# Performance work log

Measured on AMD Instinct MI355X. Metric: run time of the kernel, lower is better.

Reference implementation:

```python
import jax, jax.numpy as jnp
import numpy as np

TEMPERATURE = 0.2
EPS = 1e-12  # F.normalize clamp eps


def setup_inputs() -> dict:
    key = jax.random.key(0)
    k1, k2 = jax.random.split(key)
    N, D = 4096, 256
    Z_1 = jax.random.normal(k1, (N, D), dtype=jnp.float32)
    Z_2 = jax.random.normal(k2, (N, D), dtype=jnp.float32)
    return {"Z_1": Z_1, "Z_2": Z_2}


def reference(Z_1, Z_2):
    N = Z_1.shape[0]
    M = 2 * N
    # concat views and L2-normalize rows (torch F.normalize semantics)
    Z = jnp.concatenate([Z_1, Z_2], axis=0)  # [2N, D]
    Z = Z / jnp.maximum(jnp.linalg.norm(Z, axis=1, keepdims=True), EPS)
    # full similarity matrix [2N, 2N]
    sim = jnp.matmul(Z, Z.T) / TEMPERATURE
    # positive for row i is column (i + N) mod 2N (other view of same sample,
    # identity diagonal discarded as in create_contrastive_masks)
    idx = jnp.arange(M)
    pos = sim[idx, (idx + N) % M]  # [2N]
    # logits = [pos, negatives]; label = 0 => CE = logsumexp(pos U negs) - pos.
    # pos U negs = all columns except the identity diagonal.
    diag = idx[:, None] == idx[None, :]
    sim_masked = jnp.where(diag, -jnp.inf, sim)
    lse = jax.nn.logsumexp(sim_masked, axis=1)  # [2N]
    return jnp.mean(lse - pos)
```

## Files before the change

kernel.cpp:

```cpp
#include <hip/hip_runtime.h>
#include <cstdint>
#include <cstddef>

#define TINV 5.0f
#define C5L2E 7.2134752044448170f
#define NROWS 4096
#define DDIM 256
#define MM 8192

typedef __bf16 bf16x8 __attribute__((ext_vector_type(8)));
typedef float f32x4 __attribute__((ext_vector_type(4)));

typedef const void __attribute__((address_space(1)))* gas_ptr;
typedef void __attribute__((address_space(3)))* las_ptr;

__global__ __launch_bounds__(256, 2)
void nrm_kernel(const float* __restrict__ Z1, const float* __restrict__ Z2,
                unsigned short* __restrict__ Zb, float* __restrict__ rowsumAcc) {
    if (blockIdx.x < 32) rowsumAcc[blockIdx.x * 256 + threadIdx.x] = 0.f;
    const int w = threadIdx.x >> 6, lane = threadIdx.x & 63;
    const int row = blockIdx.x * 4 + w;
    const float* src = row < NROWS ? Z1 + (size_t)row * DDIM
                                   : Z2 + (size_t)(row - NROWS) * DDIM;
    float4 v = reinterpret_cast<const float4*>(src)[lane];
    float ss = v.x*v.x + v.y*v.y + v.z*v.z + v.w*v.w;
    #pragma unroll
    for (int m = 1; m < 64; m <<= 1) ss += __shfl_xor(ss, m, 64);
    float inv = 1.0f / fmaxf(sqrtf(ss), 1e-12f);
    float o[4] = { v.x*inv, v.y*inv, v.z*inv, v.w*inv };
    unsigned short us[4];
    #pragma unroll
    for (int e = 0; e < 4; ++e) {
        unsigned int b = __builtin_bit_cast(unsigned int, o[e]);
        b += 0x7FFFu + ((b >> 16) & 1u);
        us[e] = (unsigned short)(b >> 16);
    }
    reinterpret_cast<ushort4*>(Zb + (size_t)row * DDIM)[lane] =
        *reinterpret_cast<ushort4*>(us);
}

__device__ __forceinline__ void stage32(const unsigned short* Zb, char* ldsdst,
                                        int rowStart, int tid) {
    const char* base = reinterpret_cast<const char*>(Zb) + (size_t)rowStart * 512;
    #pragma unroll
    for (int it = 0; it < 8; ++it) {
        int L = it * 4096 + tid * 16;
        int row = L >> 9;
        int soff = row * 512 + ((L & 511) ^ ((row & 15) << 4));
        __builtin_amdgcn_global_load_lds((gas_ptr)(base + soff), (las_ptr)(ldsdst + L),
                                         16, 0, 0);
    }
}

__global__ __launch_bounds__(256, 2)
void sim_lse_kernel(const unsigned short* __restrict__ Zb,
                    float* __restrict__ rowsumAcc,
                    float* __restrict__ posArr) {
    __shared__ char lds[65536];
    __shared__ float colPartLds[4][8][64];
    const int tid = threadIdx.x;
    const int lane = tid & 63;
    const int w = tid >> 6;
    const int r15 = lane & 15, hi = lane >> 4;
    const int r = blockIdx.x >> 3;
    const int s = blockIdx.x & 7;
    const int e0 = r & 7, e1 = e0 ^ 4;
    const int nt = 8 + ((s == e0) || (s == e1));
    const int extraHalf = (s == e1) ? 1 : 0;
    const int R0 = r * 128;

    if (s == 0) {
        colPartLds[w][0][lane] = 0.f;
        colPartLds[w][1][lane] = 0.f;
    }

    int koff[8];
    #pragma unroll
    for (int kk = 0; kk < 8; ++kk)
        koff[kk] = ((hi << 4) | (kk << 6)) ^ (r15 << 4);

    stage32(Zb, lds, R0, tid);
    stage32(Zb, lds + 32768, R0 + 64, tid);
    __syncthreads();
    bf16x8 qf[2][8];
    {
        const char* ab = lds + ((w >> 1) << 15);
        #pragma unroll
        for (int mf = 0; mf < 2; ++mf)
            #pragma unroll
            for (int kk = 0; kk < 8; ++kk)
                qf[mf][kk] = *reinterpret_cast<const bf16x8*>(
                    ab + ((w & 1) * 32 + mf * 16 + r15) * 512 + koff[kk]);
    }
    __syncthreads();

    int baddr[8];
    #pragma unroll
    for (int kk = 0; kk < 8; ++kk) baddr[kk] = r15 * 512 + koff[kk];

    float rowsum[2][4] = {{0,0,0,0},{0,0,0,0}};
    const int iBase = R0 + w * 32 + (hi << 2);

    auto colOf = [&](int t) -> int {
        int d = (t < 8) ? (s + ((t >> 1) << 3)) : 32;
        int half = (t < 8) ? (t & 1) : extraHalf;
        return ((r + d) & 63) * 128 + half * 64;
    };

    stage32(Zb, lds, colOf(0), tid);

    for (int t = 0; t < nt; ++t) {
        const int C0 = colOf(t);
        const int cur = (t & 1) << 15;
        if (t < nt - 1) {
            stage32(Zb, lds + (cur ^ 32768), colOf(t + 1), tid);
            asm volatile("s_waitcnt vmcnt(8)" ::: "memory");
        } else {
            asm volatile("s_waitcnt vmcnt(0)" ::: "memory");
        }
        __builtin_amdgcn_s_barrier();
        __builtin_amdgcn_sched_barrier(0);

        const int mode = (t == 8) ? 2 : ((s == 0 && t < 2) ? 1 : 0);
        #pragma unroll
        for (int nf = 0; nf < 4; ++nf) {
            f32x4 acc0 = {0,0,0,0}, acc1 = {0,0,0,0};
            #pragma unroll
            for (int kk = 0; kk < 8; ++kk) {
                bf16x8 b = *reinterpret_cast<const bf16x8*>(lds + cur + nf * 8192 + baddr[kk]);
                acc0 = __builtin_amdgcn_mfma_f32_16x16x32_bf16(qf[0][kk], b, acc0, 0, 0, 0);
                acc1 = __builtin_amdgcn_mfma_f32_16x16x32_bf16(qf[1][kk], b, acc1, 0, 0, 0);
            }
            const int j = C0 + nf * 16 + r15;
            if (mode == 0) {
                float s8 = 0.f;
                #pragma unroll
                for (int mf = 0; mf < 2; ++mf) {
                    const f32x4 a = mf ? acc1 : acc0;
                    #pragma unroll
                    for (int rr = 0; rr < 4; ++rr) {
                        float e = __builtin_amdgcn_exp2f(fmaf(a[rr], C5L2E, -C5L2E));
                        rowsum[mf][rr] += e;
                        s8 += e;
                    }
                }
                s8 += __shfl_xor(s8, 16, 64);
                s8 += __shfl_xor(s8, 32, 64);
                if (hi == 0) colPartLds[w][t][(t & 1) * 0 + nf * 16 + r15] = s8;
            } else if (mode == 1) {
                #pragma unroll
                for (int mf = 0; mf < 2; ++mf) {
                    const f32x4 a = mf ? acc1 : acc0;
                    #pragma unroll
                    for (int rr = 0; rr < 4; ++rr) {
                        const int i = iBase + mf * 16 + rr;
                        if (j != i)
                            rowsum[mf][rr] += __builtin_amdgcn_exp2f(fmaf(a[rr], C5L2E, -C5L2E));
                    }
                }
            } else {
                #pragma unroll
                for (int mf = 0; mf < 2; ++mf) {
                    const f32x4 a = mf ? acc1 : acc0;
                    #pragma unroll
                    for (int rr = 0; rr < 4; ++rr) {
                        const int i = iBase + mf * 16 + rr;
                        rowsum[mf][rr] += __builtin_amdgcn_exp2f(fmaf(a[rr], C5L2E, -C5L2E));
                        if (j == (i ^ 4096)) posArr[i] = a[rr] * TINV;
                    }
                }
            }
        }
        asm volatile("" ::: "memory");
        __builtin_amdgcn_sched_barrier(0);
        __builtin_amdgcn_s_barrier();
    }

    __syncthreads();
    #pragma unroll
    for (int z = 0; z < 2; ++z) {
        const int idx = z * 256 + tid;
        const int tt = idx >> 6, c = idx & 63;
        float v = colPartLds[0][tt][c] + colPartLds[1][tt][c]
                + colPartLds[2][tt][c] + colPartLds[3][tt][c];
        if (v != 0.f) atomicAdd(&rowsumAcc[colOf(tt) + c], v);
    }

    #pragma unroll
    for (int mf = 0; mf < 2; ++mf)
        #pragma unroll
        for (int rr = 0; rr < 4; ++rr) {
            float v = rowsum[mf][rr];
            v += __shfl_xor(v, 1, 64);
            v += __shfl_xor(v, 2, 64);
            v += __shfl_xor(v, 4, 64);
            v += __shfl_xor(v, 8, 64);
            if (r15 == 0) atomicAdd(&rowsumAcc[iBase + mf * 16 + rr], v);
        }
}

__global__ __launch_bounds__(128)
void fin1_kernel(const float* __restrict__ rowsumAcc, const float* __restrict__ posArr,
                 float* __restrict__ blockSums) {
    const int tid = threadIdx.x;
    const int i = blockIdx.x * 128 + tid;
    double v = (double)(logf(rowsumAcc[i]) + 5.0f - posArr[i]);
    #pragma unroll
    for (int m = 1; m < 64; m <<= 1) v += __shfl_xor(v, m, 64);
    __shared__ double red[2];
    if ((tid & 63) == 0) red[tid >> 6] = v;
    __syncthreads();
    if (tid == 0) blockSums[blockIdx.x] = (float)(red[0] + red[1]);
}

__global__ __launch_bounds__(64)
void fin2_kernel(const float* __restrict__ blockSums, float* __restrict__ out) {
    double v = (double)blockSums[threadIdx.x];
    #pragma unroll
    for (int m = 1; m < 64; m <<= 1) v += __shfl_xor(v, m, 64);
    if (threadIdx.x == 0) out[0] = (float)(v / (double)MM);
}

extern "C" void kernel_launch(void* const* d_in, const int* in_sizes, int n_in,
                              void* d_out, int out_size, void* d_ws, size_t ws_size,
                              hipStream_t stream) {
    const float* Z1 = (const float*)d_in[0];
    const float* Z2 = (const float*)d_in[1];
    float* out = (float*)d_out;
    char* ws = (char*)d_ws;
    unsigned short* Zb = (unsigned short*)ws;
    float* posArr = (float*)(ws + 4194304);
    float* rowsumAcc = (float*)(ws + 4194304 + 32768);
    float* blockSums = (float*)(ws + 4194304 + 65536);

    nrm_kernel<<<MM / 4, 256, 0, stream>>>(Z1, Z2, Zb, rowsumAcc);
    sim_lse_kernel<<<64 * 8, 256, 0, stream>>>(Zb, rowsumAcc, posArr);
    fin1_kernel<<<64, 128, 0, stream>>>(rowsumAcc, posArr, blockSums);
    fin2_kernel<<<1, 64, 0, stream>>>(blockSums, out);
}
```

Before: 43.31 us.

## Retile waves to 2x2 grid with 64-row A fragments held in AGPRs

Changes the per-wave tile from 32 rows by 64 columns to 64 rows by 32 columns, arranged as a 2x2 wave grid. Each B fragment loaded from LDS now feeds four MFMAs instead of two, halving LDS reads per MFMA. The A operand (query fragments) is doubled and pinned to AGPRs through inline asm to relieve VGPR pressure. Column partial sums are reduced across two waves instead of four. The risk is higher register use under the two-blocks-per-CU launch bound, and inline asm hides the MFMA dependencies from the compiler's scheduler.

```diff
diff --git a/kernel.cpp b/kernel.cpp
--- a/kernel.cpp
+++ b/kernel.cpp
@@ -9,6 +9,7 @@
 #define MM 8192
 
 typedef __bf16 bf16x8 __attribute__((ext_vector_type(8)));
+typedef int i32x4 __attribute__((ext_vector_type(4)));
 typedef float f32x4 __attribute__((ext_vector_type(4)));
 
 typedef const void __attribute__((address_space(1)))* gas_ptr;
@@ -57,10 +58,11 @@
                     float* __restrict__ rowsumAcc,
                     float* __restrict__ posArr) {
     __shared__ char lds[65536];
-    __shared__ float colPartLds[4][8][64];
+    __shared__ float colPartLds[4][8][32];
     const int tid = threadIdx.x;
     const int lane = tid & 63;
     const int w = tid >> 6;
+    const int wr = w >> 1, wc = w & 1;
     const int r15 = lane & 15, hi = lane >> 4;
     const int r = blockIdx.x >> 3;
     const int s = blockIdx.x & 7;
@@ -69,7 +71,7 @@
     const int extraHalf = (s == e1) ? 1 : 0;
     const int R0 = r * 128;
 
-    if (s == 0) {
+    if (s == 0 && lane < 32) {
         colPartLds[w][0][lane] = 0.f;
         colPartLds[w][1][lane] = 0.f;
     }
@@ -82,24 +84,25 @@
     stage32(Zb, lds, R0, tid);
     stage32(Zb, lds + 32768, R0 + 64, tid);
     __syncthreads();
-    bf16x8 qf[2][8];
+    i32x4 qf[4][8];
     {
-        const char* ab = lds + ((w >> 1) << 15);
+        const char* ab = lds + (wr << 15);
         #pragma unroll
-        for (int mf = 0; mf < 2; ++mf)
+        for (int mf = 0; mf < 4; ++mf)
             #pragma unroll
             for (int kk = 0; kk < 8; ++kk)
-                qf[mf][kk] = *reinterpret_cast<const bf16x8*>(
-                    ab + ((w & 1) * 32 + mf * 16 + r15) * 512 + koff[kk]);
+                qf[mf][kk] = *reinterpret_cast<const i32x4*>(
+                    ab + (mf * 16 + r15) * 512 + koff[kk]);
     }
     __syncthreads();
 
     int baddr[8];
     #pragma unroll
-    for (int kk = 0; kk < 8; ++kk) baddr[kk] = r15 * 512 + koff[kk];
-
-    float rowsum[2][4] = {{0,0,0,0},{0,0,0,0}};
-    const int iBase = R0 + w * 32 + (hi << 2);
+    for (int kk = 0; kk < 8; ++kk)
+        baddr[kk] = (wc * 32 + r15) * 512 + koff[kk];
+
+    float rowsum[4][4] = {{0,0,0,0},{0,0,0,0},{0,0,0,0},{0,0,0,0}};
+    const int iBase = R0 + wr * 64 + (hi << 2);
 
     auto colOf = [&](int t) -> int {
         int d = (t < 8) ? (s + ((t >> 1) << 3)) : 32;
@@ -123,52 +126,48 @@
 
         const int mode = (t == 8) ? 2 : ((s == 0 && t < 2) ? 1 : 0);
         #pragma unroll
-        for (int nf = 0; nf < 4; ++nf) {
-            f32x4 acc0 = {0,0,0,0}, acc1 = {0,0,0,0};
+        for (int nf = 0; nf < 2; ++nf) {
+            f32x4 acc[4] = {{0,0,0,0},{0,0,0,0},{0,0,0,0},{0,0,0,0}};
             #pragma unroll
             for (int kk = 0; kk < 8; ++kk) {
-                bf16x8 b = *reinterpret_cast<const bf16x8*>(lds + cur + nf * 8192 + baddr[kk]);
-                acc0 = __builtin_amdgcn_mfma_f32_16x16x32_bf16(qf[0][kk], b, acc0, 0, 0, 0);
-                acc1 = __builtin_amdgcn_mfma_f32_16x16x32_bf16(qf[1][kk], b, acc1, 0, 0, 0);
+                i32x4 b = *reinterpret_cast<const i32x4*>(lds + cur + nf * 8192 + baddr[kk]);
+                #pragma unroll
+                for (int mf = 0; mf < 4; ++mf)
+                    asm("v_mfma_f32_16x16x32_bf16 %0, %1, %2, %0"
+                        : "+v"(acc[mf]) : "a"(qf[mf][kk]), "v"(b));
             }
-            const int j = C0 + nf * 16 + r15;
+            const int j = C0 + wc * 32 + nf * 16 + r15;
             if (mode == 0) {
                 float s8 = 0.f;
                 #pragma unroll
-                for (int mf = 0; mf < 2; ++mf) {
-                    const f32x4 a = mf ? acc1 : acc0;
+                for (int mf = 0; mf < 4; ++mf)
                     #pragma unroll
                     for (int rr = 0; rr < 4; ++rr) {
-                        float e = __builtin_amdgcn_exp2f(fmaf(a[rr], C5L2E, -C5L2E));
+                        float e = __builtin_amdgcn_exp2f(fmaf(acc[mf][rr], C5L2E, -C5L2E));
                         rowsum[mf][rr] += e;
                         s8 += e;
                     }
-                }
                 s8 += __shfl_xor(s8, 16, 64);
                 s8 += __shfl_xor(s8, 32, 64);
-                if (hi == 0) colPartLds[w][t][(t & 1) * 0 + nf * 16 + r15] = s8;
+                if (hi == 0) colPartLds[w][t][nf * 16 + r15] = s8;
             } else if (mode == 1) {
                 #pragma unroll
-                for (int mf = 0; mf < 2; ++mf) {
-                    const f32x4 a = mf ? acc1 : acc0;
+                for (int mf = 0; mf < 4; ++mf)
                     #pragma unroll
                     for (int rr = 0; rr < 4; ++rr) {
                         const int i = iBase + mf * 16 + rr;
                         if (j != i)
-                            rowsum[mf][rr] += __builtin_amdgcn_exp2f(fmaf(a[rr], C5L2E, -C5L2E));
+                            rowsum[mf][rr] += __builtin_amdgcn_exp2f(fmaf(acc[mf][rr], C5L2E, -C5L2E));
                     }
-                }
             } else {
                 #pragma unroll
-                for (int mf = 0; mf < 2; ++mf) {
-                    const f32x4 a = mf ? acc1 : acc0;
+                for (int mf = 0; mf < 4; ++mf)
                     #pragma unroll
                     for (int rr = 0; rr < 4; ++rr) {
                         const int i = iBase + mf * 16 + rr;
-                        rowsum[mf][rr] += __builtin_amdgcn_exp2f(fmaf(a[rr], C5L2E, -C5L2E));
-                        if (j == (i ^ 4096)) posArr[i] = a[rr] * TINV;
+                        rowsum[mf][rr] += __builtin_amdgcn_exp2f(fmaf(acc[mf][rr], C5L2E, -C5L2E));
+                        if (j == (i ^ 4096)) posArr[i] = acc[mf][rr] * TINV;
                     }
-                }
             }
         }
         asm volatile("" ::: "memory");
@@ -181,13 +180,13 @@
     for (int z = 0; z < 2; ++z) {
         const int idx = z * 256 + tid;
         const int tt = idx >> 6, c = idx & 63;
-        float v = colPartLds[0][tt][c] + colPartLds[1][tt][c]
-                + colPartLds[2][tt][c] + colPartLds[3][tt][c];
+        const int ww = c >> 5;
+        float v = colPartLds[ww][tt][c & 31] + colPartLds[2 + ww][tt][c & 31];
         if (v != 0.f) atomicAdd(&rowsumAcc[colOf(tt) + c], v);
     }
 
     #pragma unroll
-    for (int mf = 0; mf < 2; ++mf)
+    for (int mf = 0; mf < 4; ++mf)
         #pragma unroll
         for (int rr = 0; rr < 4; ++rr) {
             float v = rowsum[mf][rr];
```

Result: no change. 42.53 us (-1.8%).
